# Kernel optimization log

Measured on AMD Instinct MI355X. Metric: run time of the kernel, lower is better.

The kernel has to match this reference:

```python
import jax, jax.numpy as jnp
import numpy as np

B, T, IN, H, OUT = 64, 2048, 64, 512, 32


def setup_inputs() -> dict:
    key = jax.random.key(0)
    ks = jax.random.split(key, 8)
    # xavier_normal with gain=0.5: std = gain * sqrt(2/(fan_in+fan_out))
    std_fz = 0.5 * np.sqrt(2.0 / ((IN + H) + 2 * H))
    std_r = 0.5 * np.sqrt(2.0 / ((IN + H) + H))
    # nn.Linear default init: uniform(-1/sqrt(fan_in), 1/sqrt(fan_in))
    lim = 1.0 / np.sqrt(H)
    return {
        "u": jax.random.normal(ks[0], (B, T, IN), dtype=jnp.float32),
        "x0": jax.random.uniform(ks[1], (B, 1, H), dtype=jnp.float32),
        "kernel_fz": std_fz * jax.random.normal(ks[2], (IN + H, 2 * H), dtype=jnp.float32),
        "bias_fz": jnp.zeros((2 * H,), dtype=jnp.float32),
        "kernel_r": std_r * jax.random.normal(ks[3], (IN + H, H), dtype=jnp.float32),
        "bias_r": jnp.zeros((H,), dtype=jnp.float32),
        "W_out": jax.random.uniform(ks[4], (OUT, H), dtype=jnp.float32, minval=-lim, maxval=lim),
        "b_out": jax.random.uniform(ks[5], (OUT,), dtype=jnp.float32, minval=-lim, maxval=lim),
    }


def reference(u, x0, kernel_fz, bias_fz, kernel_r, bias_r, W_out, b_out):
    Hd = kernel_r.shape[1]
    x_init = x0[:, 0, :]  # [B, H]

    def step(x, u_t):
        # u_t: [B, IN], x: [B, H]
        fz = jax.nn.sigmoid(jnp.concatenate([u_t, x], axis=-1) @ kernel_fz + bias_fz)
        f, z = fz[:, :Hd], fz[:, Hd:]
        r = jnp.tanh(jnp.concatenate([u_t, f * x], axis=-1) @ kernel_r + bias_r)
        xk = (1.0 - z) * x + z * r
        y = x @ W_out.T + b_out  # output computed from PREVIOUS state, as in torch step()
        return xk, y

    u_tb = jnp.swapaxes(u, 0, 1)  # [T, B, IN]
    _, ys = jax.lax.scan(step, x_init, u_tb)  # ys: [T, B, OUT]
    return jnp.swapaxes(ys, 0, 1)  # [B, T, OUT]
```

## Files before the change

### kernel.cpp

```cpp
#include <hip/hip_runtime.h>
#include <stdint.h>

#define B_    64
#define T_    2048
#define IN_   64
#define H_    512
#define H2_   1024
#define OUT_  32
#define KTOT  576

#define NBG   8
#define NCG   32
#define NTHR  256
#define BPG   8
#define KSL   18
#define RS    12

#define FLAG_STRIDE 16
#define FLAG_WORDS  (NBG * 2 * NCG * FLAG_STRIDE)
#define ABORT_IDX   FLAG_WORDS
#define BUF_BASE    (FLAG_WORDS + 16)
#define XSLAB       32768

__device__ __forceinline__ void gpubf(float* p, float v) {
  asm volatile("global_atomic_swap %0, %1, off sc1\n\ts_waitcnt vmcnt(0)"
               :: "v"(p), "v"(v) : "memory");
}
__device__ __forceinline__ void gpubu(unsigned* p, unsigned v) {
  asm volatile("global_atomic_swap %0, %1, off sc1\n\ts_waitcnt vmcnt(0)"
               :: "v"(p), "v"(v) : "memory");
}
__device__ __forceinline__ void gload4x4(const float* p0, const float* p1,
                                         const float* p2, const float* p3,
                                         float4& a, float4& b, float4& c, float4& d) {
  asm volatile(
      "global_load_dwordx4 %0, %4, off sc0 sc1\n\t"
      "global_load_dwordx4 %1, %5, off sc0 sc1\n\t"
      "global_load_dwordx4 %2, %6, off sc0 sc1\n\t"
      "global_load_dwordx4 %3, %7, off sc0 sc1\n\t"
      "s_waitcnt vmcnt(0)"
      : "=&v"(a), "=&v"(b), "=&v"(c), "=&v"(d)
      : "v"(p0), "v"(p1), "v"(p2), "v"(p3)
      : "memory");
}

__global__ __launch_bounds__(256) void gru_init(float* ws, const float* __restrict__ x0) {
  int i = blockIdx.x * blockDim.x + threadIdx.x;
  int stride = gridDim.x * blockDim.x;
  unsigned* w = (unsigned*)ws;
  for (int k = i; k < BUF_BASE; k += stride) w[k] = 0u;
  for (int k = i; k < NBG * H_ * BPG; k += stride) {
    int bg = k >> 12, j = (k >> 3) & (H_ - 1), b = k & 7;
    ws[BUF_BASE + k] = x0[(bg * 8 + b) * H_ + j];
  }
}

__device__ __forceinline__ void gbar_arrive(unsigned* flags, int slot, unsigned target) {
  __syncthreads();
  if (threadIdx.x == 0) gpubu(flags + slot, target);
}

__device__ __forceinline__ bool gbar_wait(unsigned* flags, int base, unsigned target,
                                          unsigned* abort_w) {
  __shared__ int s_ok;
  const int tid = threadIdx.x;
  int ok = 1;
  if (tid < NCG) {
    const unsigned* f = flags + base + tid * FLAG_STRIDE;
    int polls = 0;
    while (__hip_atomic_load(f, __ATOMIC_RELAXED, __HIP_MEMORY_SCOPE_AGENT) < target) {
      __builtin_amdgcn_s_sleep(1);
      if ((++polls & 255) == 0) {
        if (__hip_atomic_load(abort_w, __ATOMIC_RELAXED, __HIP_MEMORY_SCOPE_AGENT) != 0u ||
            polls > 2000000) {
          __hip_atomic_store(abort_w, 1u, __ATOMIC_RELAXED, __HIP_MEMORY_SCOPE_AGENT);
          ok = 0;
          break;
        }
      }
    }
  }
  if (tid < 64) {
    unsigned long long bad = __ballot(ok == 0);
    if (tid == 0) s_ok = (bad == 0ull) ? 1 : 0;
  }
  __syncthreads();
  __atomic_signal_fence(__ATOMIC_ACQUIRE);
  return s_ok != 0;
}

__global__ __launch_bounds__(NTHR, 1) void gru_main(
    const float* __restrict__ u, const float* __restrict__ kfz,
    const float* __restrict__ bfz, const float* __restrict__ kr,
    const float* __restrict__ br, const float* __restrict__ wout,
    const float* __restrict__ bout, float* __restrict__ out, float* ws) {
  unsigned* flags = (unsigned*)ws;
  unsigned* abort_w = flags + ABORT_IDX;
  float* xg0 = ws + BUF_BASE;
  float* xg1 = xg0 + XSLAB;
  float* xfg = xg1 + XSLAB;

  const int bg  = blockIdx.x & 7;
  const int cg  = blockIdx.x >> 3;
  const int tid = threadIdx.x;
  const int w   = tid >> 6;
  const int l   = tid & 63;
  const int cq  = l & 7;
  const int g   = l >> 3;
  const int kb  = (w * 8 + g) * KSL;
  const int fc  = tid >> 3;
  const int fb  = tid & 7;
  const int yb  = tid >> 5;
  const int yq  = tid & 31;

  const int slotA = ((bg * 2 + 0) * NCG + cg) * FLAG_STRIDE;
  const int slotB = ((bg * 2 + 1) * NCG + cg) * FLAG_STRIDE;
  const int baseA = (bg * 2 + 0) * NCG * FLAG_STRIDE;
  const int baseB = (bg * 2 + 1) * NCG * FLAG_STRIDE;

  __shared__ float bufA[KTOT * RS];
  __shared__ float pA[4 * 32 * RS];
  __shared__ float pB[4 * 16 * RS];
  __shared__ float rbuf[16 * 8];

  float wA[KSL][4];
#pragma unroll
  for (int i = 0; i < KSL; ++i)
#pragma unroll
    for (int m = 0; m < 4; ++m) {
      int c = 4 * cq + m;
      int gcol = (c < 16) ? (16 * cg + c) : (512 + 16 * cg + (c - 16));
      wA[i][m] = kfz[(size_t)(kb + i) * H2_ + gcol];
    }
  float wB[KSL][2];
#pragma unroll
  for (int i = 0; i < KSL; ++i)
#pragma unroll
    for (int m = 0; m < 2; ++m)
      wB[i][m] = kr[(size_t)(kb + i) * H_ + (16 * cg + 2 * cq + m)];
  float wy[16];
#pragma unroll
  for (int i = 0; i < 16; ++i) wy[i] = wout[cg * H_ + (yq + 32 * i)];
  const float by = bout[cg];
  const int fzc = (fc < 16) ? (16 * cg + fc) : (512 + 16 * cg + (fc - 16));
  const float biasA = bfz[fzc];
  const float biasB = (tid < 128) ? br[16 * cg + fc] : 0.0f;

  float zreg = 0.0f, xoldz = 0.0f;

  {
    int k2 = tid & 31, b = tid >> 5;
    float2 uv = *(const float2*)&u[((size_t)(bg * 8 + b) * T_) * IN_ + 2 * k2];
    bufA[(2 * k2) * RS + b] = uv.x;
    bufA[(2 * k2 + 1) * RS + b] = uv.y;
  }

  for (int t = 0; t < T_; ++t) {
    float* xcur = (t & 1) ? xg1 : xg0;
    float* xnxt = (t & 1) ? xg0 : xg1;

    {
      const float* s0 = &xcur[(size_t)(bg * H_ + tid) * 8];
      const float* s2 = &xcur[(size_t)(bg * H_ + tid + 256) * 8];
      float4 a, b, c, d;
      gload4x4(s0, s0 + 4, s2, s2 + 4, a, b, c, d);
      *(float4*)&bufA[(64 + tid) * RS] = a;
      *(float4*)&bufA[(64 + tid) * RS + 4] = b;
      *(float4*)&bufA[(64 + tid + 256) * RS] = c;
      *(float4*)&bufA[(64 + tid + 256) * RS + 4] = d;
    }
    __syncthreads();

    float acc[4][8] = {};
#pragma unroll
    for (int i = 0; i < KSL; ++i) {
      const float* xr = &bufA[(kb + i) * RS];
      float4 x0 = *(const float4*)xr;
      float4 x1 = *(const float4*)(xr + 4);
#pragma unroll
      for (int m = 0; m < 4; ++m) {
        float wv = wA[i][m];
        acc[m][0] += wv * x0.x; acc[m][1] += wv * x0.y;
        acc[m][2] += wv * x0.z; acc[m][3] += wv * x0.w;
        acc[m][4] += wv * x1.x; acc[m][5] += wv * x1.y;
        acc[m][6] += wv * x1.z; acc[m][7] += wv * x1.w;
      }
    }

#pragma unroll
    for (int m = 0; m < 4; ++m)
#pragma unroll
      for (int b = 0; b < 8; ++b) {
        acc[m][b] += __shfl_xor(acc[m][b], 8);
        acc[m][b] += __shfl_xor(acc[m][b], 16);
        acc[m][b] += __shfl_xor(acc[m][b], 32);
      }
    if (g == 0) {
#pragma unroll
      for (int m = 0; m < 4; ++m) {
        float* p = &pA[(w * 32 + 4 * cq + m) * RS];
        *(float4*)p = make_float4(acc[m][0], acc[m][1], acc[m][2], acc[m][3]);
        *(float4*)(p + 4) = make_float4(acc[m][4], acc[m][5], acc[m][6], acc[m][7]);
      }
    }
    __syncthreads();

    {
      float s = pA[(0 * 32 + fc) * RS + fb] + pA[(1 * 32 + fc) * RS + fb] +
                pA[(2 * 32 + fc) * RS + fb] + pA[(3 * 32 + fc) * RS + fb] + biasA;
      float sig = 1.0f / (1.0f + __expf(-s));
      if (fc < 16) {
        float xo = bufA[(64 + 16 * cg + fc) * RS + fb];
        gpubf(&xfg[(size_t)(bg * H_ + 16 * cg + fc) * 8 + fb], sig * xo);
      } else {
        zreg = sig;
        xoldz = bufA[(64 + 16 * cg + (fc - 16)) * RS + fb];
      }
    }

    gbar_arrive(flags, slotA, (unsigned)(t + 1));

    {
      float yp = 0.0f;
#pragma unroll
      for (int i = 0; i < 16; ++i)
        yp += wy[i] * bufA[(64 + yq + 32 * i) * RS + yb];
      yp += __shfl_xor(yp, 1);  yp += __shfl_xor(yp, 2);
      yp += __shfl_xor(yp, 4);  yp += __shfl_xor(yp, 8);
      yp += __shfl_xor(yp, 16);
      if (yq == 0)
        out[((size_t)(bg * 8 + yb) * T_ + t) * OUT_ + cg] = yp + by;
    }

    if (!gbar_wait(flags, baseA, (unsigned)(t + 1), abort_w)) return;

    {
      const float* s0 = &xfg[(size_t)(bg * H_ + tid) * 8];
      const float* s2 = &xfg[(size_t)(bg * H_ + tid + 256) * 8];
      float4 a, b, c, d;
      gload4x4(s0, s0 + 4, s2, s2 + 4, a, b, c, d);
      *(float4*)&bufA[(64 + tid) * RS] = a;
      *(float4*)&bufA[(64 + tid) * RS + 4] = b;
      *(float4*)&bufA[(64 + tid + 256) * RS] = c;
      *(float4*)&bufA[(64 + tid + 256) * RS + 4] = d;
    }
    __syncthreads();

    float acc2[2][8] = {};
#pragma unroll
    for (int i = 0; i < KSL; ++i) {
      const float* xr = &bufA[(kb + i) * RS];
      float4 x0 = *(const float4*)xr;
      float4 x1 = *(const float4*)(xr + 4);
#pragma unroll
      for (int m = 0; m < 2; ++m) {
        float wv = wB[i][m];
        acc2[m][0] += wv * x0.x; acc2[m][1] += wv * x0.y;
        acc2[m][2] += wv * x0.z; acc2[m][3] += wv * x0.w;
        acc2[m][4] += wv * x1.x; acc2[m][5] += wv * x1.y;
        acc2[m][6] += wv * x1.z; acc2[m][7] += wv * x1.w;
      }
    }
#pragma unroll
    for (int m = 0; m < 2; ++m)
#pragma unroll
      for (int b = 0; b < 8; ++b) {
        acc2[m][b] += __shfl_xor(acc2[m][b], 8);
        acc2[m][b] += __shfl_xor(acc2[m][b], 16);
        acc2[m][b] += __shfl_xor(acc2[m][b], 32);
      }
    if (g == 0) {
#pragma unroll
      for (int m = 0; m < 2; ++m) {
        float* p = &pB[(w * 16 + 2 * cq + m) * RS];
        *(float4*)p = make_float4(acc2[m][0], acc2[m][1], acc2[m][2], acc2[m][3]);
        *(float4*)(p + 4) = make_float4(acc2[m][4], acc2[m][5], acc2[m][6], acc2[m][7]);
      }
    }
    __syncthreads();

    if (tid < 128) {
      float s = pB[(0 * 16 + fc) * RS + fb] + pB[(1 * 16 + fc) * RS + fb] +
                pB[(2 * 16 + fc) * RS + fb] + pB[(3 * 16 + fc) * RS + fb] + biasB;
      float e = __expf(2.0f * s);
      rbuf[fc * 8 + fb] = 1.0f - 2.0f / (1.0f + e);
    }
    __syncthreads();

    if (tid >= 128) {
      float r = rbuf[(fc - 16) * 8 + fb];
      float xn = xoldz + zreg * (r - xoldz);
      gpubf(&xnxt[(size_t)(bg * H_ + 16 * cg + (fc - 16)) * 8 + fb], xn);
    }

    gbar_arrive(flags, slotB, (unsigned)(t + 1));

    if (t + 1 < T_) {
      int k2 = tid & 31, b = tid >> 5;
      float2 uv = *(const float2*)&u[((size_t)(bg * 8 + b) * T_ + (t + 1)) * IN_ + 2 * k2];
      bufA[(2 * k2) * RS + b] = uv.x;
      bufA[(2 * k2 + 1) * RS + b] = uv.y;
    }

    if (!gbar_wait(flags, baseB, (unsigned)(t + 1), abort_w)) return;
  }
}

extern "C" void kernel_launch(void* const* d_in, const int* in_sizes, int n_in,
                              void* d_out, int out_size, void* d_ws, size_t ws_size,
                              hipStream_t stream) {
  const float* u    = (const float*)d_in[0];
  const float* x0   = (const float*)d_in[1];
  const float* kfz  = (const float*)d_in[2];
  const float* bfz  = (const float*)d_in[3];
  const float* kr   = (const float*)d_in[4];
  const float* br   = (const float*)d_in[5];
  const float* wout = (const float*)d_in[6];
  const float* bout = (const float*)d_in[7];
  float* out = (float*)d_out;
  float* ws  = (float*)d_ws;

  hipLaunchKernelGGL(gru_init, dim3(64), dim3(256), 0, stream, ws, x0);
  hipLaunchKernelGGL(gru_main, dim3(NBG * NCG), dim3(NTHR), 0, stream,
                     u, kfz, bfz, kr, br, wout, bout, out, ws);
}
```

Measured before the change: 15.26 ms.

## Replace flag barriers with epoch-tagged 64-bit data publishes and polling

Each published value is written with an atomic 64-bit swap that pairs the float with a step-epoch tag, so consumers poll the data slab directly until every tag matches instead of waiting on separate per-block arrival flags. This removes the arrive/wait barrier round-trips, the per-store waitcnt, and the extra flag traffic on each of the two sync points per step. In exchange it doubles the bytes of the exchange buffers, and every thread re-reads whole slabs while polling, which can add memory traffic under contention.

Result: slower. 15.85 ms (+3.9%).

```diff
diff --git a/kernel.cpp b/kernel.cpp
--- a/kernel.cpp
+++ b/kernel.cpp
@@ -16,32 +16,57 @@
 #define KSL   18
 #define RS    12
 
-#define FLAG_STRIDE 16
-#define FLAG_WORDS  (NBG * 2 * NCG * FLAG_STRIDE)
-#define ABORT_IDX   FLAG_WORDS
-#define BUF_BASE    (FLAG_WORDS + 16)
-#define XSLAB       32768
-
-__device__ __forceinline__ void gpubf(float* p, float v) {
-  asm volatile("global_atomic_swap %0, %1, off sc1\n\ts_waitcnt vmcnt(0)"
-               :: "v"(p), "v"(v) : "memory");
-}
-__device__ __forceinline__ void gpubu(unsigned* p, unsigned v) {
-  asm volatile("global_atomic_swap %0, %1, off sc1\n\ts_waitcnt vmcnt(0)"
-               :: "v"(p), "v"(v) : "memory");
-}
-__device__ __forceinline__ void gload4x4(const float* p0, const float* p1,
-                                         const float* p2, const float* p3,
-                                         float4& a, float4& b, float4& c, float4& d) {
-  asm volatile(
-      "global_load_dwordx4 %0, %4, off sc0 sc1\n\t"
-      "global_load_dwordx4 %1, %5, off sc0 sc1\n\t"
-      "global_load_dwordx4 %2, %6, off sc0 sc1\n\t"
-      "global_load_dwordx4 %3, %7, off sc0 sc1\n\t"
-      "s_waitcnt vmcnt(0)"
-      : "=&v"(a), "=&v"(b), "=&v"(c), "=&v"(d)
-      : "v"(p0), "v"(p1), "v"(p2), "v"(p3)
-      : "memory");
+#define ABORT_IDX 0
+#define BUF_BASE  16
+#define PAIRS_BG  (H_ * BPG)
+#define PSLAB     (NBG * PAIRS_BG * 2)
+
+__device__ __forceinline__ void gpub2(float* p, float v, unsigned e) {
+  unsigned long long q =
+      ((unsigned long long)e << 32) | (unsigned long long)__float_as_uint(v);
+  asm volatile("global_atomic_swap_x2 %0, %1, off sc1"
+               :: "v"(p), "v"(q) : "memory");
+}
+
+__device__ __forceinline__ bool poll_slab(
+    const float* b0, const float* b1, unsigned target, unsigned* abort_w,
+    float4& r0, float4& r1, float4& r2, float4& r3,
+    float4& r4, float4& r5, float4& r6, float4& r7) {
+  int polls = 0;
+  for (;;) {
+    asm volatile(
+        "global_load_dwordx4 %0, %8, off sc0 sc1\n\t"
+        "global_load_dwordx4 %1, %8, off offset:16 sc0 sc1\n\t"
+        "global_load_dwordx4 %2, %8, off offset:32 sc0 sc1\n\t"
+        "global_load_dwordx4 %3, %8, off offset:48 sc0 sc1\n\t"
+        "global_load_dwordx4 %4, %9, off sc0 sc1\n\t"
+        "global_load_dwordx4 %5, %9, off offset:16 sc0 sc1\n\t"
+        "global_load_dwordx4 %6, %9, off offset:32 sc0 sc1\n\t"
+        "global_load_dwordx4 %7, %9, off offset:48 sc0 sc1\n\t"
+        "s_waitcnt vmcnt(0)"
+        : "=&v"(r0), "=&v"(r1), "=&v"(r2), "=&v"(r3),
+          "=&v"(r4), "=&v"(r5), "=&v"(r6), "=&v"(r7)
+        : "v"(b0), "v"(b1)
+        : "memory");
+    unsigned m =
+        (__float_as_uint(r0.y) ^ target) | (__float_as_uint(r0.w) ^ target) |
+        (__float_as_uint(r1.y) ^ target) | (__float_as_uint(r1.w) ^ target) |
+        (__float_as_uint(r2.y) ^ target) | (__float_as_uint(r2.w) ^ target) |
+        (__float_as_uint(r3.y) ^ target) | (__float_as_uint(r3.w) ^ target) |
+        (__float_as_uint(r4.y) ^ target) | (__float_as_uint(r4.w) ^ target) |
+        (__float_as_uint(r5.y) ^ target) | (__float_as_uint(r5.w) ^ target) |
+        (__float_as_uint(r6.y) ^ target) | (__float_as_uint(r6.w) ^ target) |
+        (__float_as_uint(r7.y) ^ target) | (__float_as_uint(r7.w) ^ target);
+    if (m == 0u) return true;
+    __builtin_amdgcn_s_sleep(1);
+    if ((++polls & 63) == 0) {
+      if (__hip_atomic_load(abort_w, __ATOMIC_RELAXED, __HIP_MEMORY_SCOPE_AGENT) != 0u ||
+          polls > 300000) {
+        __hip_atomic_store(abort_w, 1u, __ATOMIC_RELAXED, __HIP_MEMORY_SCOPE_AGENT);
+        return false;
+      }
+    }
+  }
 }
 
 __global__ __launch_bounds__(256) void gru_init(float* ws, const float* __restrict__ x0) {
@@ -49,44 +74,13 @@
   int stride = gridDim.x * blockDim.x;
   unsigned* w = (unsigned*)ws;
   for (int k = i; k < BUF_BASE; k += stride) w[k] = 0u;
-  for (int k = i; k < NBG * H_ * BPG; k += stride) {
-    int bg = k >> 12, j = (k >> 3) & (H_ - 1), b = k & 7;
-    ws[BUF_BASE + k] = x0[(bg * 8 + b) * H_ + j];
+  unsigned* rest = w + BUF_BASE + PSLAB;
+  for (int k = i; k < 2 * PSLAB; k += stride) rest[k] = 0u;
+  for (int p = i; p < NBG * PAIRS_BG; p += stride) {
+    int bg = p >> 12, col = (p >> 3) & (H_ - 1), b = p & 7;
+    ws[BUF_BASE + 2 * p] = x0[(bg * 8 + b) * H_ + col];
+    w[BUF_BASE + 2 * p + 1] = 0u;
   }
-}
-
-__device__ __forceinline__ void gbar_arrive(unsigned* flags, int slot, unsigned target) {
-  __syncthreads();
-  if (threadIdx.x == 0) gpubu(flags + slot, target);
-}
-
-__device__ __forceinline__ bool gbar_wait(unsigned* flags, int base, unsigned target,
-                                          unsigned* abort_w) {
-  __shared__ int s_ok;
-  const int tid = threadIdx.x;
-  int ok = 1;
-  if (tid < NCG) {
-    const unsigned* f = flags + base + tid * FLAG_STRIDE;
-    int polls = 0;
-    while (__hip_atomic_load(f, __ATOMIC_RELAXED, __HIP_MEMORY_SCOPE_AGENT) < target) {
-      __builtin_amdgcn_s_sleep(1);
-      if ((++polls & 255) == 0) {
-        if (__hip_atomic_load(abort_w, __ATOMIC_RELAXED, __HIP_MEMORY_SCOPE_AGENT) != 0u ||
-            polls > 2000000) {
-          __hip_atomic_store(abort_w, 1u, __ATOMIC_RELAXED, __HIP_MEMORY_SCOPE_AGENT);
-          ok = 0;
-          break;
-        }
-      }
-    }
-  }
-  if (tid < 64) {
-    unsigned long long bad = __ballot(ok == 0);
-    if (tid == 0) s_ok = (bad == 0ull) ? 1 : 0;
-  }
-  __syncthreads();
-  __atomic_signal_fence(__ATOMIC_ACQUIRE);
-  return s_ok != 0;
 }
 
 __global__ __launch_bounds__(NTHR, 1) void gru_main(
@@ -94,11 +88,10 @@
     const float* __restrict__ bfz, const float* __restrict__ kr,
     const float* __restrict__ br, const float* __restrict__ wout,
     const float* __restrict__ bout, float* __restrict__ out, float* ws) {
-  unsigned* flags = (unsigned*)ws;
-  unsigned* abort_w = flags + ABORT_IDX;
-  float* xg0 = ws + BUF_BASE;
-  float* xg1 = xg0 + XSLAB;
-  float* xfg = xg1 + XSLAB;
+  unsigned* abort_w = (unsigned*)ws + ABORT_IDX;
+  float* xg0p = ws + BUF_BASE;
+  float* xg1p = xg0p + PSLAB;
+  float* xfgp = xg1p + PSLAB;
 
   const int bg  = blockIdx.x & 7;
   const int cg  = blockIdx.x >> 3;
@@ -113,15 +106,11 @@
   const int yb  = tid >> 5;
   const int yq  = tid & 31;
 
-  const int slotA = ((bg * 2 + 0) * NCG + cg) * FLAG_STRIDE;
-  const int slotB = ((bg * 2 + 1) * NCG + cg) * FLAG_STRIDE;
-  const int baseA = (bg * 2 + 0) * NCG * FLAG_STRIDE;
-  const int baseB = (bg * 2 + 1) * NCG * FLAG_STRIDE;
-
   __shared__ float bufA[KTOT * RS];
   __shared__ float pA[4 * 32 * RS];
   __shared__ float pB[4 * 16 * RS];
   __shared__ float rbuf[16 * 8];
+  __shared__ int s_bad;
 
   float wA[KSL][4];
 #pragma unroll
@@ -148,26 +137,32 @@
 
   float zreg = 0.0f, xoldz = 0.0f;
 
+  if (tid == 0) s_bad = 0;
   {
     int k2 = tid & 31, b = tid >> 5;
     float2 uv = *(const float2*)&u[((size_t)(bg * 8 + b) * T_) * IN_ + 2 * k2];
     bufA[(2 * k2) * RS + b] = uv.x;
     bufA[(2 * k2 + 1) * RS + b] = uv.y;
   }
+  __syncthreads();
 
   for (int t = 0; t < T_; ++t) {
-    float* xcur = (t & 1) ? xg1 : xg0;
-    float* xnxt = (t & 1) ? xg0 : xg1;
+    const float* xcp = (t & 1) ? xg1p : xg0p;
+    float*       xnp = (t & 1) ? xg0p : xg1p;
 
     {
-      const float* s0 = &xcur[(size_t)(bg * H_ + tid) * 8];
-      const float* s2 = &xcur[(size_t)(bg * H_ + tid + 256) * 8];
-      float4 a, b, c, d;
-      gload4x4(s0, s0 + 4, s2, s2 + 4, a, b, c, d);
-      *(float4*)&bufA[(64 + tid) * RS] = a;
-      *(float4*)&bufA[(64 + tid) * RS + 4] = b;
-      *(float4*)&bufA[(64 + tid + 256) * RS] = c;
-      *(float4*)&bufA[(64 + tid + 256) * RS + 4] = d;
+      const float* b0 = xcp + 2 * ((size_t)bg * PAIRS_BG + (size_t)tid * 8);
+      const float* b1 = b0 + 4096;
+      float4 r0, r1, r2, r3, r4, r5, r6, r7;
+      bool ok = poll_slab(b0, b1, (unsigned)t, abort_w,
+                          r0, r1, r2, r3, r4, r5, r6, r7);
+      if (!ok) s_bad = 1;
+      __syncthreads();
+      if (s_bad) return;
+      *(float4*)&bufA[(64 + tid) * RS]       = make_float4(r0.x, r0.z, r1.x, r1.z);
+      *(float4*)&bufA[(64 + tid) * RS + 4]   = make_float4(r2.x, r2.z, r3.x, r3.z);
+      *(float4*)&bufA[(64 + tid + 256) * RS]     = make_float4(r4.x, r4.z, r5.x, r5.z);
+      *(float4*)&bufA[(64 + tid + 256) * RS + 4] = make_float4(r6.x, r6.z, r7.x, r7.z);
     }
     __syncthreads();
 
@@ -211,14 +206,13 @@
       float sig = 1.0f / (1.0f + __expf(-s));
       if (fc < 16) {
         float xo = bufA[(64 + 16 * cg + fc) * RS + fb];
-        gpubf(&xfg[(size_t)(bg * H_ + 16 * cg + fc) * 8 + fb], sig * xo);
+        float* p = &xfgp[2 * ((size_t)bg * PAIRS_BG + (size_t)(16 * cg + fc) * 8 + fb)];
+        gpub2(p, sig * xo, (unsigned)(t + 1));
       } else {
         zreg = sig;
         xoldz = bufA[(64 + 16 * cg + (fc - 16)) * RS + fb];
       }
     }
-
-    gbar_arrive(flags, slotA, (unsigned)(t + 1));
 
     {
       float yp = 0.0f;
@@ -232,17 +226,19 @@
         out[((size_t)(bg * 8 + yb) * T_ + t) * OUT_ + cg] = yp + by;
     }
 
-    if (!gbar_wait(flags, baseA, (unsigned)(t + 1), abort_w)) return;
-
     {
-      const float* s0 = &xfg[(size_t)(bg * H_ + tid) * 8];
-      const float* s2 = &xfg[(size_t)(bg * H_ + tid + 256) * 8];
-      float4 a, b, c, d;
-      gload4x4(s0, s0 + 4, s2, s2 + 4, a, b, c, d);
-      *(float4*)&bufA[(64 + tid) * RS] = a;
-      *(float4*)&bufA[(64 + tid) * RS + 4] = b;
-      *(float4*)&bufA[(64 + tid + 256) * RS] = c;
-      *(float4*)&bufA[(64 + tid + 256) * RS + 4] = d;
+      const float* b0 = xfgp + 2 * ((size_t)bg * PAIRS_BG + (size_t)tid * 8);
+      const float* b1 = b0 + 4096;
+      float4 r0, r1, r2, r3, r4, r5, r6, r7;
+      bool ok = poll_slab(b0, b1, (unsigned)(t + 1), abort_w,
+                          r0, r1, r2, r3, r4, r5, r6, r7);
+      if (!ok) s_bad = 1;
+      __syncthreads();
+      if (s_bad) return;
+      *(float4*)&bufA[(64 + tid) * RS]       = make_float4(r0.x, r0.z, r1.x, r1.z);
+      *(float4*)&bufA[(64 + tid) * RS + 4]   = make_float4(r2.x, r2.z, r3.x, r3.z);
+      *(float4*)&bufA[(64 + tid + 256) * RS]     = make_float4(r4.x, r4.z, r5.x, r5.z);
+      *(float4*)&bufA[(64 + tid + 256) * RS + 4] = make_float4(r6.x, r6.z, r7.x, r7.z);
     }
     __syncthreads();
 
@@ -290,19 +286,15 @@
     if (tid >= 128) {
       float r = rbuf[(fc - 16) * 8 + fb];
       float xn = xoldz + zreg * (r - xoldz);
-      gpubf(&xnxt[(size_t)(bg * H_ + 16 * cg + (fc - 16)) * 8 + fb], xn);
-    }
-
-    gbar_arrive(flags, slotB, (unsigned)(t + 1));
-
+      float* p = &xnp[2 * ((size_t)bg * PAIRS_BG + (size_t)(16 * cg + (fc - 16)) * 8 + fb)];
+      gpub2(p, xn, (unsigned)(t + 1));
+    }
     if (t + 1 < T_) {
       int k2 = tid & 31, b = tid >> 5;
       float2 uv = *(const float2*)&u[((size_t)(bg * 8 + b) * T_ + (t + 1)) * IN_ + 2 * k2];
       bufA[(2 * k2) * RS + b] = uv.x;
       bufA[(2 * k2 + 1) * RS + b] = uv.y;
     }
-
-    if (!gbar_wait(flags, baseB, (unsigned)(t + 1), abort_w)) return;
   }
 }
 
```
